# Performance work log

Hardware: AMD Instinct MI355X
Metric: run time of the kernel (lower is better)

The kernel has to match this reference:

```python
import jax, jax.numpy as jnp
import numpy as np

N = 50000   # nodes
E = 800000  # directed edges (self-loops added inside reference)
F_IN, H, C = 128, 96, 32


def setup_inputs() -> dict:
    key = jax.random.key(0)
    ks = jax.random.split(key, 8)
    x = jax.random.normal(ks[0], (N, F_IN), dtype=jnp.float32)
    edge_index = jax.random.randint(ks[1], (2, E), 0, N, dtype=jnp.int64)
    W1 = jax.random.normal(ks[2], (F_IN, H), dtype=jnp.float32) * 0.05
    b1 = jnp.zeros((H,), dtype=jnp.float32)
    W2 = jax.random.normal(ks[3], (H, H), dtype=jnp.float32) * 0.05
    b2 = jnp.zeros((H,), dtype=jnp.float32)
    W3 = jax.random.normal(ks[4], (H, C), dtype=jnp.float32) * 0.05
    b3 = jnp.zeros((C,), dtype=jnp.float32)
    return {"x": x, "edge_index": edge_index, "W1": W1, "b1": b1,
            "W2": W2, "b2": b2, "W3": W3, "b3": b3}


def gcn_conv(x, W, b, src, dst, n):
    """PyG GCNConv: x' = D^{-1/2} (A+I) D^{-1/2} (x W) + b (self-loops in src/dst)."""
    xw = x @ W                                        # [n, out]
    ones = jnp.ones(src.shape[0], dtype=xw.dtype)
    deg = jax.ops.segment_sum(ones, dst, num_segments=n)
    dinv = jnp.where(deg > 0, jax.lax.rsqrt(jnp.maximum(deg, 1.0)), 0.0)
    norm = dinv[src] * dinv[dst]                      # [E+n]
    msg = norm[:, None] * xw[src]                     # gather + scale
    out = jax.ops.segment_sum(msg, dst, num_segments=n)  # scatter-add
    return out + b


def reference(x, edge_index, W1, b1, W2, b2, W3, b3):
    loop = jnp.arange(N, dtype=edge_index.dtype)
    src = jnp.concatenate([edge_index[0], loop])      # add self-loops once
    dst = jnp.concatenate([edge_index[1], loop])
    h = jax.nn.relu(gcn_conv(x, W1, b1, src, dst, N))   # dropout is identity (eval)
    h = jax.nn.relu(gcn_conv(h, W2, b2, src, dst, N))
    h = gcn_conv(h, W3, b3, src, dst, N)
    return jax.nn.log_softmax(h, axis=1)
```

## Files before the change

### kernel.cpp

```cpp
#include <hip/hip_runtime.h>
#include <hip/hip_fp16.h>


typedef _Float16 half8 __attribute__((ext_vector_type(8)));
typedef float f32x4 __attribute__((ext_vector_type(4)));

constexpr int CAP = 64;
constexpr int NPB = 128;
constexpr int NBINS_P = 512;
constexpr int EPB = 4096;
constexpr int BCAP = 2560;

__device__ inline __half2 h2u(unsigned int u) {
    union { unsigned int x; __half2 h; } c;
    c.x = u;
    return c.h;
}
__device__ inline unsigned int u_h2(__half2 h) {
    union { __half2 h; unsigned int x; } c;
    c.h = h;
    return c.x;
}

__device__ inline int ext8(uint4 p, int j) {
    unsigned int h = (j & 4) ? ((j & 2) ? p.w : p.z) : ((j & 2) ? p.y : p.x);
    return (j & 1) ? (int)(h >> 16) : (int)(h & 0xFFFFu);
}

__global__ __launch_bounds__(256) void prep_kernel(const int* __restrict__ ei, int twoE,
                                                   int* __restrict__ flags,
                                                   int* __restrict__ bin_cnt,
                                                   const float* __restrict__ W1,
                                                   const float* __restrict__ W2,
                                                   const float* __restrict__ W3,
                                                   __half* __restrict__ Wt1,
                                                   __half* __restrict__ Wt2,
                                                   __half* __restrict__ Wt3) {
    if (blockIdx.x == 0) {
        if (threadIdx.x < 8) flags[threadIdx.x] = 0;
        for (int b = threadIdx.x; b < NBINS_P; b += 256) bin_cnt[b] = 0;
        __syncthreads();
        int c = 0;
        for (int j = threadIdx.x; j < 2048 && j < twoE; j += 256) {
            if ((j & 1) && ei[j] != 0) c++;
        }
        if (c) atomicAdd(&flags[4], c);
        return;
    }
    int i = (blockIdx.x - 1) * 256 + threadIdx.x;
    if (i < 128 * 96) {
        int f = i / 128, k = i - f * 128;
        Wt1[i] = __float2half(W1[(size_t)k * 96 + f]);
    } else if (i < 128 * 96 + 96 * 96) {
        int j = i - 128 * 96;
        int f = j / 96, k = j - f * 96;
        Wt2[j] = __float2half(W2[(size_t)k * 96 + f]);
    } else if (i < 128 * 96 + 96 * 96 + 96 * 32) {
        int j = i - 128 * 96 - 96 * 96;
        int f = j / 96, k = j - f * 96;
        Wt3[j] = __float2half(W3[(size_t)k * 32 + f]);
    }
}

__device__ inline int ld_idx(const int* ei, int half_, int i, int E, bool i64) {
    return i64 ? ei[2 * (half_ * (size_t)E + i)] : ei[half_ * (size_t)E + i];
}

__global__ __launch_bounds__(256) void part_kernel(const int* __restrict__ ei,
                                                   const int* __restrict__ flags,
                                                   int* __restrict__ bin_cnt,
                                                   int* __restrict__ bins, int E, int n) {
    __shared__ int hist[NBINS_P], excl[NBINS_P], cur[NBINS_P], gpos[NBINS_P];
    __shared__ int tmp[256];
    __shared__ int stage[EPB];
    const int tid = threadIdx.x;
    const bool i64 = (flags[4] == 0);
    for (int b = tid; b < NBINS_P; b += 256) hist[b] = 0;
    __syncthreads();

    int v[EPB / 256];
    const int base = blockIdx.x * EPB;
#pragma unroll
    for (int j = 0; j < EPB / 256; j++) {
        int i = base + j * 256 + tid;
        v[j] = -1;
        if (i < E) {
            int s = ld_idx(ei, 0, i, E, i64);
            int d = ld_idx(ei, 1, i, E, i64);
            if ((unsigned)s < (unsigned)n && (unsigned)d < (unsigned)n) {
                int bin = d >> 7, ln = d & 127;
                v[j] = (bin << 23) | (ln << 16) | s;
                atomicAdd(&hist[bin], 1);
            }
        }
    }
    __syncthreads();
    int a0 = hist[2 * tid], a1 = hist[2 * tid + 1];
    int pairsum = a0 + a1;
    tmp[tid] = pairsum;
    __syncthreads();
    for (int off = 1; off < 256; off <<= 1) {
        int t = (tid >= off) ? tmp[tid - off] : 0;
        __syncthreads();
        tmp[tid] += t;
        __syncthreads();
    }
    int S = tmp[tid] - pairsum;
    excl[2 * tid] = S;
    excl[2 * tid + 1] = S + a0;
    cur[2 * tid] = S;
    cur[2 * tid + 1] = S + a0;
    __syncthreads();
    for (int b = tid; b < NBINS_P; b += 256)
        gpos[b] = hist[b] ? atomicAdd(&bin_cnt[b], hist[b]) : 0;
#pragma unroll
    for (int j = 0; j < EPB / 256; j++) {
        if (v[j] != -1) {
            int bin = ((unsigned)v[j]) >> 23;
            int p = atomicAdd(&cur[bin], 1);
            stage[p] = v[j];
        }
    }
    __syncthreads();
    int total = excl[NBINS_P - 1] + hist[NBINS_P - 1];
    for (int i = tid; i < total; i += 256) {
        int w = stage[i];
        int bin = ((unsigned)w) >> 23;
        int k = gpos[bin] + (i - excl[bin]);
        if (k < BCAP) bins[(size_t)bin * BCAP + k] = w;
    }
}

__global__ __launch_bounds__(256) void build_kernel(const int* __restrict__ bin_cnt,
                                                    const int* __restrict__ bins,
                                                    int* __restrict__ cnt,
                                                    unsigned short* __restrict__ csr, int n) {
    __shared__ unsigned short lcsr[NPB * CAP];
    __shared__ int lcnt[NPB];
    const int b = blockIdx.x, tid = threadIdx.x;
    for (int i = tid; i < NPB; i += 256) lcnt[i] = 0;
    __syncthreads();
    int m = min(bin_cnt[b], BCAP);
    for (int i = tid; i < m; i += 256) {
        int w = bins[(size_t)b * BCAP + i];
        int ln = (w >> 16) & 127;
        int p = atomicAdd(&lcnt[ln], 1);
        if (p < CAP) lcsr[ln * CAP + p] = (unsigned short)(w & 0xFFFF);
    }
    __syncthreads();
    const int node0 = b * NPB;
    const unsigned int* l32 = (const unsigned int*)lcsr;
    unsigned int* c32 = (unsigned int*)(csr + (size_t)node0 * CAP);
    for (int i = tid; i < NPB * CAP / 2; i += 256) {
        int node = node0 + (i >> 5);
        if (node < n) c32[i] = l32[i];
    }
    for (int t = tid; t < NPB; t += 256)
        if (node0 + t < n) cnt[node0 + t] = lcnt[t];
}

__device__ inline half8 to_h8(float4 u0, float4 u1) {
    half8 r;
    r[0] = (_Float16)u0.x; r[1] = (_Float16)u0.y; r[2] = (_Float16)u0.z; r[3] = (_Float16)u0.w;
    r[4] = (_Float16)u1.x; r[5] = (_Float16)u1.y; r[6] = (_Float16)u1.z; r[7] = (_Float16)u1.w;
    return r;
}

template <int K, int F, bool XF32>
__global__ __launch_bounds__(256) void gemm_mfma(const void* __restrict__ X,
                                                 const __half* __restrict__ Wt,
                                                 const int* __restrict__ cnt,
                                                 __half* __restrict__ out, int n) {
    constexpr int KP = K + 8;
    constexpr int FT = F / 16;
    constexpr int KC = K / 32;
    __shared__ _Float16 Wl[F * KP];
    for (int i = threadIdx.x; i < F * (K / 8); i += 256) {
        int f = i / (K / 8), c = i - f * (K / 8);
        *(half8*)&Wl[f * KP + c * 8] = *(const half8*)&Wt[(size_t)f * K + c * 8];
    }
    __syncthreads();
    const int wave = threadIdx.x >> 6, lane = threadIdx.x & 63;
    const int node0 = (blockIdx.x * 4 + wave) * 16;
    if (node0 >= n) return;
    const int m = lane & 15, q = lane >> 4;
    const int arow = min(node0 + m, n - 1);

    half8 af[KC];
    if (XF32) {
        const float* xp = (const float*)X + (size_t)arow * K + q * 8;
#pragma unroll
        for (int kc = 0; kc < KC; kc++) {
            float4 u0 = *(const float4*)(xp + kc * 32);
            float4 u1 = *(const float4*)(xp + kc * 32 + 4);
            af[kc] = to_h8(u0, u1);
        }
    } else {
        const __half* xp = (const __half*)X + (size_t)arow * K + q * 8;
#pragma unroll
        for (int kc = 0; kc < KC; kc++) af[kc] = *(const half8*)(xp + kc * 32);
    }

    f32x4 acc[FT];
#pragma unroll
    for (int t = 0; t < FT; t++) acc[t] = (f32x4)0.f;
#pragma unroll
    for (int kc = 0; kc < KC; kc++) {
#pragma unroll
        for (int t = 0; t < FT; t++) {
            half8 b = *(const half8*)&Wl[(t * 16 + m) * KP + kc * 32 + q * 8];
            acc[t] = __builtin_amdgcn_mfma_f32_16x16x32_f16(af[kc], b, acc[t], 0, 0, 0);
        }
    }
    float dv[4];
#pragma unroll
    for (int r = 0; r < 4; r++) {
        int node = node0 + q * 4 + r;
        dv[r] = (node < n) ? rsqrtf(1.0f + (float)cnt[node]) : 0.f;
    }
#pragma unroll
    for (int t = 0; t < FT; t++)
#pragma unroll
        for (int r = 0; r < 4; r++) {
            int node = node0 + q * 4 + r;
            if (node < n) {
                float vv = acc[t][r] * dv[r];
                out[(size_t)node * F + t * 16 + m] = __float2half(vv);
            }
        }
}

__global__ __launch_bounds__(256) void agg96_f16(const __half* __restrict__ xws,
                                                 const int* __restrict__ cnt,
                                                 const unsigned short* __restrict__ csr,
                                                 const float* __restrict__ bias,
                                                 __half* __restrict__ out, int n) {
    int node = blockIdx.x * 4 + (threadIdx.x >> 6);
    int lane = threadIdx.x & 63;
    if (node >= n) return;
    const int g = lane < 24 ? 0 : 1;
    const int c = g ? lane - 24 : lane;
    const bool act = lane < 48;
    int deg = cnt[node];
    int m = min(deg, CAP);
    float dv = rsqrtf(1.0f + (float)deg);
    const uint4* r4 = (const uint4*)(csr + (size_t)node * CAP);
    const unsigned int* r2 = (const unsigned int*)r4;
    __half2 a0 = h2u(0u), a1 = h2u(0u);
    if (lane < 24) {
        uint2 s = *(const uint2*)(xws + (size_t)node * 96 + c * 4);
        a0 = h2u(s.x);
        a1 = h2u(s.y);
    }
    int e = 0;
#define A96_U(pr_) (g ? ((pr_) >> 16) : ((pr_) & 0xFFFFu))
#define A96_LD(u_) (*(const uint2*)(xws + (size_t)(u_) * 96 + c * 4))
#define A96_ACC(w_) { a0 = __hadd2(a0, h2u((w_).x)); a1 = __hadd2(a1, h2u((w_).y)); }
    for (; e + 16 <= m; e += 16) {
        uint4 pa = r4[e >> 3], pb = r4[(e >> 3) + 1];
        if (act) {
            uint2 w0 = A96_LD(A96_U(pa.x)), w1 = A96_LD(A96_U(pa.y));
            uint2 w2 = A96_LD(A96_U(pa.z)), w3 = A96_LD(A96_U(pa.w));
            uint2 w4 = A96_LD(A96_U(pb.x)), w5 = A96_LD(A96_U(pb.y));
            uint2 w6 = A96_LD(A96_U(pb.z)), w7 = A96_LD(A96_U(pb.w));
            A96_ACC(w0) A96_ACC(w1) A96_ACC(w2) A96_ACC(w3)
            A96_ACC(w4) A96_ACC(w5) A96_ACC(w6) A96_ACC(w7)
        }
    }
    if (e + 8 <= m) {
        uint4 pa = r4[e >> 3];
        if (act) {
            uint2 w0 = A96_LD(A96_U(pa.x)), w1 = A96_LD(A96_U(pa.y));
            uint2 w2 = A96_LD(A96_U(pa.z)), w3 = A96_LD(A96_U(pa.w));
            A96_ACC(w0) A96_ACC(w1) A96_ACC(w2) A96_ACC(w3)
        }
        e += 8;
    }
    if (e + 4 <= m) {
        unsigned int p0 = r2[e >> 1], p1 = r2[(e >> 1) + 1];
        if (act) {
            uint2 w0 = A96_LD(A96_U(p0)), w1 = A96_LD(A96_U(p1));
            A96_ACC(w0) A96_ACC(w1)
        }
        e += 4;
    }
    if (e + 2 <= m) {
        unsigned int p0 = r2[e >> 1];
        if (act) {
            uint2 w0 = A96_LD(A96_U(p0));
            A96_ACC(w0)
        }
        e += 2;
    }
    if (e < m && lane < 24) {
        int u = ((const unsigned short*)r4)[e];
        uint2 w0 = A96_LD(u);
        A96_ACC(w0)
    }
#undef A96_U
#undef A96_LD
#undef A96_ACC
    unsigned int p0 = __shfl((int)u_h2(a0), lane + 24);
    unsigned int p1 = __shfl((int)u_h2(a1), lane + 24);
    if (lane < 24) {
        a0 = __hadd2(a0, h2u(p0));
        a1 = __hadd2(a1, h2u(p1));
        float2 f0 = __half22float2(a0);
        float2 f1 = __half22float2(a1);
        float4 bb = *(const float4*)&bias[c * 4];
        float r0 = fmaxf(fmaf(dv, f0.x, bb.x), 0.f);
        float r1 = fmaxf(fmaf(dv, f0.y, bb.y), 0.f);
        float r2v = fmaxf(fmaf(dv, f1.x, bb.z), 0.f);
        float r3 = fmaxf(fmaf(dv, f1.y, bb.w), 0.f);
        union { __half2 h[2]; uint2 u; } pk;
        pk.h[0] = __floats2half2_rn(r0, r1);
        pk.h[1] = __floats2half2_rn(r2v, r3);
        *(uint2*)(out + (size_t)node * 96 + c * 4) = pk.u;
    }
}

__global__ __launch_bounds__(256) void agg32_lsm(const __half* __restrict__ xws,
                                                 const int* __restrict__ cnt,
                                                 const unsigned short* __restrict__ csr,
                                                 const float* __restrict__ bias,
                                                 float* __restrict__ out, int n) {
    int node = blockIdx.x * 4 + (threadIdx.x >> 6);
    int lane = threadIdx.x & 63;
    if (node >= n) return;
    const int g = lane >> 4, l = lane & 15;
    int deg = cnt[node];
    int m = min(deg, CAP);
    float dv = rsqrtf(1.0f + (float)deg);
    const uint4* r4 = (const uint4*)(csr + (size_t)node * CAP);
    __half2 a = h2u(0u);
    if (g == 0) a = *(const __half2*)(xws + (size_t)node * 32 + l * 2);
    int e = 0;
    for (; e + 16 <= m; e += 16) {
        uint4 pa = r4[e >> 3], pb = r4[(e >> 3) + 1];
        int u0 = ext8(pa, g), u1 = ext8(pa, g + 4);
        int u2 = ext8(pb, g), u3 = ext8(pb, g + 4);
        __half2 f0 = *(const __half2*)(xws + (size_t)u0 * 32 + l * 2);
        __half2 f1 = *(const __half2*)(xws + (size_t)u1 * 32 + l * 2);
        __half2 f2 = *(const __half2*)(xws + (size_t)u2 * 32 + l * 2);
        __half2 f3 = *(const __half2*)(xws + (size_t)u3 * 32 + l * 2);
        a = __hadd2(a, __hadd2(__hadd2(f0, f1), __hadd2(f2, f3)));
    }
    if (e + 8 <= m) {
        uint4 pa = r4[e >> 3];
        int u0 = ext8(pa, g), u1 = ext8(pa, g + 4);
        __half2 f0 = *(const __half2*)(xws + (size_t)u0 * 32 + l * 2);
        __half2 f1 = *(const __half2*)(xws + (size_t)u1 * 32 + l * 2);
        a = __hadd2(a, __hadd2(f0, f1));
        e += 8;
    }
    if (e + 4 <= m) {
        unsigned int p0 = ((const unsigned int*)r4)[e >> 1];
        unsigned int p1 = ((const unsigned int*)r4)[(e >> 1) + 1];
        unsigned int h = (g & 2) ? p1 : p0;
        int u = (g & 1) ? (int)(h >> 16) : (int)(h & 0xFFFF);
        a = __hadd2(a, *(const __half2*)(xws + (size_t)u * 32 + l * 2));
        e += 4;
    }
    for (; e < m; e++) {
        if (g == 0) {
            int u = ((const unsigned short*)r4)[e];
            a = __hadd2(a, *(const __half2*)(xws + (size_t)u * 32 + l * 2));
        }
    }
    a = __hadd2(a, h2u((unsigned int)__shfl_xor((int)u_h2(a), 16)));
    a = __hadd2(a, h2u((unsigned int)__shfl_xor((int)u_h2(a), 32)));
    if (g == 0) {
        float2 av = __half22float2(a);
        float2 b = *(const float2*)&bias[l * 2];
        float rx = fmaf(dv, av.x, b.x), ry = fmaf(dv, av.y, b.y);
        float mx = fmaxf(rx, ry);
        mx = fmaxf(mx, __shfl_xor(mx, 1));
        mx = fmaxf(mx, __shfl_xor(mx, 2));
        mx = fmaxf(mx, __shfl_xor(mx, 4));
        mx = fmaxf(mx, __shfl_xor(mx, 8));
        float s = expf(rx - mx) + expf(ry - mx);
        s += __shfl_xor(s, 1);
        s += __shfl_xor(s, 2);
        s += __shfl_xor(s, 4);
        s += __shfl_xor(s, 8);
        float ls = logf(s);
        ((float2*)out)[(size_t)node * 16 + l] = {rx - mx - ls, ry - mx - ls};
    }
}

extern "C" void kernel_launch(void* const* d_in, const int* in_sizes, int n_in,
                              void* d_out, int out_size, void* d_ws, size_t ws_size,
                              hipStream_t stream) {
    const float* x  = (const float*)d_in[0];
    const int*   ei = (const int*)d_in[1];
    const float* W1 = (const float*)d_in[2];
    const float* b1 = (const float*)d_in[3];
    const float* W2 = (const float*)d_in[4];
    const float* b2 = (const float*)d_in[5];
    const float* W3 = (const float*)d_in[6];
    const float* b3 = (const float*)d_in[7];
    float* out = (float*)d_out;

    const int N_ = in_sizes[0] / 128;
    const int E_ = in_sizes[1] / 2;
    const int NBINS = (N_ + NPB - 1) / NPB;

    char* base = (char*)d_ws;
    size_t off = 0;
    auto take = [&](size_t bytes) {
        void* p = base + off;
        off = (off + bytes + 255) & ~(size_t)255;
        return p;
    };
    int*    flags   = (int*)take(4 * 8);
    int*    bin_cnt = (int*)take(4 * NBINS_P);
    int*    bins    = (int*)take(4 * (size_t)NBINS * BCAP);
    int*    cnt     = (int*)take(4 * (size_t)N_);
    unsigned short* csr = (unsigned short*)take(2 * (size_t)N_ * CAP);
    __half* Wt1     = (__half*)take(2 * 128 * 96);
    __half* Wt2     = (__half*)take(2 * 96 * 96);
    __half* Wt3     = (__half*)take(2 * 96 * 32);
    __half* bufA    = (__half*)take(2 * (size_t)N_ * 96);
    __half* bufB    = (__half*)take(2 * (size_t)N_ * 96);

    const int prepBlocks = 1 + (128 * 96 + 96 * 96 + 96 * 32 + 255) / 256;
    prep_kernel<<<prepBlocks, 256, 0, stream>>>(ei, in_sizes[1], flags, bin_cnt,
                                                W1, W2, W3, Wt1, Wt2, Wt3);
    part_kernel<<<(E_ + EPB - 1) / EPB, 256, 0, stream>>>(ei, flags, bin_cnt, bins, E_, N_);
    build_kernel<<<NBINS, 256, 0, stream>>>(bin_cnt, bins, cnt, csr, N_);

    const int gGemm = (N_ + 63) / 64;
    const int gAgg  = (N_ + 3) / 4;

    gemm_mfma<128, 96, true><<<gGemm, 256, 0, stream>>>(x, Wt1, cnt, bufA, N_);
    agg96_f16<<<gAgg, 256, 0, stream>>>(bufA, cnt, csr, b1, bufB, N_);
    gemm_mfma<96, 96, false><<<gGemm, 256, 0, stream>>>(bufB, Wt2, cnt, bufA, N_);
    agg96_f16<<<gAgg, 256, 0, stream>>>(bufA, cnt, csr, b2, bufB, N_);
    gemm_mfma<96, 32, false><<<gGemm, 256, 0, stream>>>(bufB, Wt3, cnt, bufA, N_);
    agg32_lsm<<<gAgg, 256, 0, stream>>>(bufA, cnt, csr, b3, out, N_);
}
```

Measured before the change: 219.9 us.

## Replace two-pass binned CSR build with direct atomic scatter; unroll aggregation gathers

Drops the partition-into-bins and per-bin build kernels and builds the CSR in one scatter kernel that bumps the per-node count with a global atomic and writes the source index into a fixed-capacity slot. The aggregation kernels now load the first 32 neighbour indices up front and do a fully unrolled, predicated gather for them, falling back to a simple loop beyond 32. This removes a kernel launch and the intermediate bin buffer, and avoids branchy tail handling. In exchange it adds global atomic contention and scattered 2-byte writes, and makes neighbour order nondeterministic, which can change fp16 summation order.

After: 251.0 us. 14.1% more time.

```diff
diff --git a/kernel.cpp b/kernel.cpp
--- a/kernel.cpp
+++ b/kernel.cpp
@@ -6,10 +6,6 @@
 typedef float f32x4 __attribute__((ext_vector_type(4)));
 
 constexpr int CAP = 64;
-constexpr int NPB = 128;
-constexpr int NBINS_P = 512;
-constexpr int EPB = 4096;
-constexpr int BCAP = 2560;
 
 __device__ inline __half2 h2u(unsigned int u) {
     union { unsigned int x; __half2 h; } c;
@@ -22,23 +18,22 @@
     return c.x;
 }
 
-__device__ inline int ext8(uint4 p, int j) {
-    unsigned int h = (j & 4) ? ((j & 2) ? p.w : p.z) : ((j & 2) ? p.y : p.x);
-    return (j & 1) ? (int)(h >> 16) : (int)(h & 0xFFFFu);
+__device__ inline unsigned int u4c(uint4 p, int j) {
+    return (j & 2) ? ((j & 1) ? p.w : p.z) : ((j & 1) ? p.y : p.x);
 }
 
 __global__ __launch_bounds__(256) void prep_kernel(const int* __restrict__ ei, int twoE,
                                                    int* __restrict__ flags,
-                                                   int* __restrict__ bin_cnt,
+                                                   int* __restrict__ cnt, int n,
                                                    const float* __restrict__ W1,
                                                    const float* __restrict__ W2,
                                                    const float* __restrict__ W3,
                                                    __half* __restrict__ Wt1,
                                                    __half* __restrict__ Wt2,
                                                    __half* __restrict__ Wt3) {
+    for (int i = blockIdx.x * 256 + threadIdx.x; i < n; i += gridDim.x * 256) cnt[i] = 0;
     if (blockIdx.x == 0) {
         if (threadIdx.x < 8) flags[threadIdx.x] = 0;
-        for (int b = threadIdx.x; b < NBINS_P; b += 256) bin_cnt[b] = 0;
         __syncthreads();
         int c = 0;
         for (int j = threadIdx.x; j < 2048 && j < twoE; j += 256) {
@@ -66,97 +61,38 @@
     return i64 ? ei[2 * (half_ * (size_t)E + i)] : ei[half_ * (size_t)E + i];
 }
 
-__global__ __launch_bounds__(256) void part_kernel(const int* __restrict__ ei,
-                                                   const int* __restrict__ flags,
-                                                   int* __restrict__ bin_cnt,
-                                                   int* __restrict__ bins, int E, int n) {
-    __shared__ int hist[NBINS_P], excl[NBINS_P], cur[NBINS_P], gpos[NBINS_P];
-    __shared__ int tmp[256];
-    __shared__ int stage[EPB];
-    const int tid = threadIdx.x;
+__global__ __launch_bounds__(256) void scatter_kernel(const int* __restrict__ ei,
+                                                      const int* __restrict__ flags,
+                                                      int* __restrict__ cnt,
+                                                      unsigned short* __restrict__ csr,
+                                                      int E, int n) {
     const bool i64 = (flags[4] == 0);
-    for (int b = tid; b < NBINS_P; b += 256) hist[b] = 0;
-    __syncthreads();
-
-    int v[EPB / 256];
-    const int base = blockIdx.x * EPB;
-#pragma unroll
-    for (int j = 0; j < EPB / 256; j++) {
-        int i = base + j * 256 + tid;
-        v[j] = -1;
-        if (i < E) {
-            int s = ld_idx(ei, 0, i, E, i64);
-            int d = ld_idx(ei, 1, i, E, i64);
-            if ((unsigned)s < (unsigned)n && (unsigned)d < (unsigned)n) {
-                int bin = d >> 7, ln = d & 127;
-                v[j] = (bin << 23) | (ln << 16) | s;
-                atomicAdd(&hist[bin], 1);
-            }
-        }
-    }
-    __syncthreads();
-    int a0 = hist[2 * tid], a1 = hist[2 * tid + 1];
-    int pairsum = a0 + a1;
-    tmp[tid] = pairsum;
-    __syncthreads();
-    for (int off = 1; off < 256; off <<= 1) {
-        int t = (tid >= off) ? tmp[tid - off] : 0;
-        __syncthreads();
-        tmp[tid] += t;
-        __syncthreads();
-    }
-    int S = tmp[tid] - pairsum;
-    excl[2 * tid] = S;
-    excl[2 * tid + 1] = S + a0;
-    cur[2 * tid] = S;
-    cur[2 * tid + 1] = S + a0;
-    __syncthreads();
-    for (int b = tid; b < NBINS_P; b += 256)
-        gpos[b] = hist[b] ? atomicAdd(&bin_cnt[b], hist[b]) : 0;
-#pragma unroll
-    for (int j = 0; j < EPB / 256; j++) {
-        if (v[j] != -1) {
-            int bin = ((unsigned)v[j]) >> 23;
-            int p = atomicAdd(&cur[bin], 1);
-            stage[p] = v[j];
-        }
-    }
-    __syncthreads();
-    int total = excl[NBINS_P - 1] + hist[NBINS_P - 1];
-    for (int i = tid; i < total; i += 256) {
-        int w = stage[i];
-        int bin = ((unsigned)w) >> 23;
-        int k = gpos[bin] + (i - excl[bin]);
-        if (k < BCAP) bins[(size_t)bin * BCAP + k] = w;
-    }
-}
-
-__global__ __launch_bounds__(256) void build_kernel(const int* __restrict__ bin_cnt,
-                                                    const int* __restrict__ bins,
-                                                    int* __restrict__ cnt,
-                                                    unsigned short* __restrict__ csr, int n) {
-    __shared__ unsigned short lcsr[NPB * CAP];
-    __shared__ int lcnt[NPB];
-    const int b = blockIdx.x, tid = threadIdx.x;
-    for (int i = tid; i < NPB; i += 256) lcnt[i] = 0;
-    __syncthreads();
-    int m = min(bin_cnt[b], BCAP);
-    for (int i = tid; i < m; i += 256) {
-        int w = bins[(size_t)b * BCAP + i];
-        int ln = (w >> 16) & 127;
-        int p = atomicAdd(&lcnt[ln], 1);
-        if (p < CAP) lcsr[ln * CAP + p] = (unsigned short)(w & 0xFFFF);
-    }
-    __syncthreads();
-    const int node0 = b * NPB;
-    const unsigned int* l32 = (const unsigned int*)lcsr;
-    unsigned int* c32 = (unsigned int*)(csr + (size_t)node0 * CAP);
-    for (int i = tid; i < NPB * CAP / 2; i += 256) {
-        int node = node0 + (i >> 5);
-        if (node < n) c32[i] = l32[i];
-    }
-    for (int t = tid; t < NPB; t += 256)
-        if (node0 + t < n) cnt[node0 + t] = lcnt[t];
+    const int t = blockIdx.x * 256 + threadIdx.x;
+    const int i0 = t * 2;
+    if (i0 >= E) return;
+    int s0, s1 = -1, d0, d1 = -1;
+    if (i0 + 1 < E) {
+        if (i64) {
+            int4 sv = ((const int4*)ei)[t];
+            int4 dv = ((const int4*)(ei + 2 * (size_t)E))[t];
+            s0 = sv.x; s1 = sv.z; d0 = dv.x; d1 = dv.z;
+        } else {
+            int2 sv = ((const int2*)ei)[t];
+            int2 dv = ((const int2*)(ei + (size_t)E))[t];
+            s0 = sv.x; s1 = sv.y; d0 = dv.x; d1 = dv.y;
+        }
+    } else {
+        s0 = ld_idx(ei, 0, i0, E, i64);
+        d0 = ld_idx(ei, 1, i0, E, i64);
+    }
+    if ((unsigned)s0 < (unsigned)n && (unsigned)d0 < (unsigned)n) {
+        int p = atomicAdd(&cnt[d0], 1);
+        if (p < CAP) csr[(size_t)d0 * CAP + p] = (unsigned short)s0;
+    }
+    if (s1 >= 0 && (unsigned)s1 < (unsigned)n && (unsigned)d1 < (unsigned)n) {
+        int p = atomicAdd(&cnt[d1], 1);
+        if (p < CAP) csr[(size_t)d1 * CAP + p] = (unsigned short)s1;
+    }
 }
 
 __device__ inline half8 to_h8(float4 u0, float4 u1) {
@@ -241,65 +177,41 @@
     const int g = lane < 24 ? 0 : 1;
     const int c = g ? lane - 24 : lane;
     const bool act = lane < 48;
+    const int cc = act ? c : 0;
+    const uint4* r4 = (const uint4*)(csr + (size_t)node * CAP);
+    const unsigned int* r2 = (const unsigned int*)r4;
+    uint4 P0 = r4[0], P1 = r4[1], P2 = r4[2], P3 = r4[3];
     int deg = cnt[node];
     int m = min(deg, CAP);
+    const int mm = min(m, 32);
     float dv = rsqrtf(1.0f + (float)deg);
-    const uint4* r4 = (const uint4*)(csr + (size_t)node * CAP);
-    const unsigned int* r2 = (const unsigned int*)r4;
     __half2 a0 = h2u(0u), a1 = h2u(0u);
     if (lane < 24) {
         uint2 s = *(const uint2*)(xws + (size_t)node * 96 + c * 4);
         a0 = h2u(s.x);
         a1 = h2u(s.y);
     }
-    int e = 0;
-#define A96_U(pr_) (g ? ((pr_) >> 16) : ((pr_) & 0xFFFFu))
-#define A96_LD(u_) (*(const uint2*)(xws + (size_t)(u_) * 96 + c * 4))
-#define A96_ACC(w_) { a0 = __hadd2(a0, h2u((w_).x)); a1 = __hadd2(a1, h2u((w_).y)); }
-    for (; e + 16 <= m; e += 16) {
-        uint4 pa = r4[e >> 3], pb = r4[(e >> 3) + 1];
-        if (act) {
-            uint2 w0 = A96_LD(A96_U(pa.x)), w1 = A96_LD(A96_U(pa.y));
-            uint2 w2 = A96_LD(A96_U(pa.z)), w3 = A96_LD(A96_U(pa.w));
-            uint2 w4 = A96_LD(A96_U(pb.x)), w5 = A96_LD(A96_U(pb.y));
-            uint2 w6 = A96_LD(A96_U(pb.z)), w7 = A96_LD(A96_U(pb.w));
-            A96_ACC(w0) A96_ACC(w1) A96_ACC(w2) A96_ACC(w3)
-            A96_ACC(w4) A96_ACC(w5) A96_ACC(w6) A96_ACC(w7)
-        }
-    }
-    if (e + 8 <= m) {
-        uint4 pa = r4[e >> 3];
-        if (act) {
-            uint2 w0 = A96_LD(A96_U(pa.x)), w1 = A96_LD(A96_U(pa.y));
-            uint2 w2 = A96_LD(A96_U(pa.z)), w3 = A96_LD(A96_U(pa.w));
-            A96_ACC(w0) A96_ACC(w1) A96_ACC(w2) A96_ACC(w3)
-        }
-        e += 8;
-    }
-    if (e + 4 <= m) {
-        unsigned int p0 = r2[e >> 1], p1 = r2[(e >> 1) + 1];
-        if (act) {
-            uint2 w0 = A96_LD(A96_U(p0)), w1 = A96_LD(A96_U(p1));
-            A96_ACC(w0) A96_ACC(w1)
-        }
-        e += 4;
-    }
-    if (e + 2 <= m) {
-        unsigned int p0 = r2[e >> 1];
-        if (act) {
-            uint2 w0 = A96_LD(A96_U(p0));
-            A96_ACC(w0)
-        }
-        e += 2;
-    }
-    if (e < m && lane < 24) {
-        int u = ((const unsigned short*)r4)[e];
-        uint2 w0 = A96_LD(u);
-        A96_ACC(w0)
-    }
-#undef A96_U
-#undef A96_LD
-#undef A96_ACC
+    const int gs = g * 16;
+#pragma unroll
+    for (int j = 0; j < 16; j++) {
+        unsigned int word = (j < 4) ? u4c(P0, j) :
+                            (j < 8) ? u4c(P1, j - 4) :
+                            (j < 12) ? u4c(P2, j - 8) : u4c(P3, j - 12);
+        bool sel = act && (2 * j + g) < mm;
+        int u = sel ? (int)((word >> gs) & 0xFFFFu) : node;
+        uint2 w = *(const uint2*)(xws + (size_t)u * 96 + cc * 4);
+        a0 = __hadd2(a0, h2u(sel ? w.x : 0u));
+        a1 = __hadd2(a1, h2u(sel ? w.y : 0u));
+    }
+    for (int e = 32; e < m; e += 2) {
+        unsigned int pw = r2[e >> 1];
+        if (act && (e + g) < m) {
+            int u = (int)((pw >> gs) & 0xFFFFu);
+            uint2 w = *(const uint2*)(xws + (size_t)u * 96 + cc * 4);
+            a0 = __hadd2(a0, h2u(w.x));
+            a1 = __hadd2(a1, h2u(w.y));
+        }
+    }
     unsigned int p0 = __shfl((int)u_h2(a0), lane + 24);
     unsigned int p1 = __shfl((int)u_h2(a1), lane + 24);
     if (lane < 24) {
@@ -328,42 +240,33 @@
     int lane = threadIdx.x & 63;
     if (node >= n) return;
     const int g = lane >> 4, l = lane & 15;
+    const uint4* r4 = (const uint4*)(csr + (size_t)node * CAP);
+    const unsigned int* r2 = (const unsigned int*)r4;
+    uint4 P0 = r4[0], P1 = r4[1], P2 = r4[2], P3 = r4[3];
     int deg = cnt[node];
     int m = min(deg, CAP);
+    const int mm = min(m, 32);
     float dv = rsqrtf(1.0f + (float)deg);
-    const uint4* r4 = (const uint4*)(csr + (size_t)node * CAP);
     __half2 a = h2u(0u);
     if (g == 0) a = *(const __half2*)(xws + (size_t)node * 32 + l * 2);
-    int e = 0;
-    for (; e + 16 <= m; e += 16) {
-        uint4 pa = r4[e >> 3], pb = r4[(e >> 3) + 1];
-        int u0 = ext8(pa, g), u1 = ext8(pa, g + 4);
-        int u2 = ext8(pb, g), u3 = ext8(pb, g + 4);
-        __half2 f0 = *(const __half2*)(xws + (size_t)u0 * 32 + l * 2);
-        __half2 f1 = *(const __half2*)(xws + (size_t)u1 * 32 + l * 2);
-        __half2 f2 = *(const __half2*)(xws + (size_t)u2 * 32 + l * 2);
-        __half2 f3 = *(const __half2*)(xws + (size_t)u3 * 32 + l * 2);
-        a = __hadd2(a, __hadd2(__hadd2(f0, f1), __hadd2(f2, f3)));
-    }
-    if (e + 8 <= m) {
-        uint4 pa = r4[e >> 3];
-        int u0 = ext8(pa, g), u1 = ext8(pa, g + 4);
-        __half2 f0 = *(const __half2*)(xws + (size_t)u0 * 32 + l * 2);
-        __half2 f1 = *(const __half2*)(xws + (size_t)u1 * 32 + l * 2);
-        a = __hadd2(a, __hadd2(f0, f1));
-        e += 8;
-    }
-    if (e + 4 <= m) {
-        unsigned int p0 = ((const unsigned int*)r4)[e >> 1];
-        unsigned int p1 = ((const unsigned int*)r4)[(e >> 1) + 1];
-        unsigned int h = (g & 2) ? p1 : p0;
-        int u = (g & 1) ? (int)(h >> 16) : (int)(h & 0xFFFF);
-        a = __hadd2(a, *(const __half2*)(xws + (size_t)u * 32 + l * 2));
-        e += 4;
-    }
-    for (; e < m; e++) {
-        if (g == 0) {
-            int u = ((const unsigned short*)r4)[e];
+    const int gs = (g & 1) * 16;
+    const int ghi = g >> 1;
+#pragma unroll
+    for (int j = 0; j < 8; j++) {
+        uint4 P = (j < 2) ? P0 : (j < 4) ? P1 : (j < 6) ? P2 : P3;
+        unsigned int wA = u4c(P, (2 * j) & 3);
+        unsigned int wB = u4c(P, (2 * j + 1) & 3);
+        unsigned int word = ghi ? wB : wA;
+        bool sel = (4 * j + g) < mm;
+        int u = sel ? (int)((word >> gs) & 0xFFFFu) : node;
+        __half2 f = *(const __half2*)(xws + (size_t)u * 32 + l * 2);
+        a = __hadd2(a, sel ? f : h2u(0u));
+    }
+    for (int e = 32; e < m; e += 4) {
+        unsigned int w0 = r2[e >> 1], w1 = r2[(e >> 1) + 1];
+        if ((e + g) < m) {
+            unsigned int word = ghi ? w1 : w0;
+            int u = (int)((word >> gs) & 0xFFFFu);
             a = __hadd2(a, *(const __half2*)(xws + (size_t)u * 32 + l * 2));
         }
     }
@@ -403,7 +306,6 @@
 
     const int N_ = in_sizes[0] / 128;
     const int E_ = in_sizes[1] / 2;
-    const int NBINS = (N_ + NPB - 1) / NPB;
 
     char* base = (char*)d_ws;
     size_t off = 0;
@@ -413,8 +315,6 @@
         return p;
     };
     int*    flags   = (int*)take(4 * 8);
-    int*    bin_cnt = (int*)take(4 * NBINS_P);
-    int*    bins    = (int*)take(4 * (size_t)NBINS * BCAP);
     int*    cnt     = (int*)take(4 * (size_t)N_);
     unsigned short* csr = (unsigned short*)take(2 * (size_t)N_ * CAP);
     __half* Wt1     = (__half*)take(2 * 128 * 96);
@@ -424,10 +324,9 @@
     __half* bufB    = (__half*)take(2 * (size_t)N_ * 96);
 
     const int prepBlocks = 1 + (128 * 96 + 96 * 96 + 96 * 32 + 255) / 256;
-    prep_kernel<<<prepBlocks, 256, 0, stream>>>(ei, in_sizes[1], flags, bin_cnt,
+    prep_kernel<<<prepBlocks, 256, 0, stream>>>(ei, in_sizes[1], flags, cnt, N_,
                                                 W1, W2, W3, Wt1, Wt2, Wt3);
-    part_kernel<<<(E_ + EPB - 1) / EPB, 256, 0, stream>>>(ei, flags, bin_cnt, bins, E_, N_);
-    build_kernel<<<NBINS, 256, 0, stream>>>(bin_cnt, bins, cnt, csr, N_);
+    scatter_kernel<<<(E_ + 511) / 512, 256, 0, stream>>>(ei, flags, cnt, csr, E_, N_);
 
     const int gGemm = (N_ + 63) / 64;
     const int gAgg  = (N_ + 3) / 4;
```
